# Optimization experiments

Hardware: AMD Instinct MI355X
Metric: run time of the kernel (lower is better)

## Reference

```python
import jax, jax.numpy as jnp
import numpy as np

EPS = 1e-5  # torch BatchNorm1d default eps


def setup_inputs() -> dict:
    key = jax.random.key(0)
    ks = jax.random.split(key, 8)
    F, P = 32, 64            # frames, peds per frame
    B = F * P                # batch = 2048
    E, H, M, D = 64, 128, 512, 1024  # embed, h_dim, pool_mlp_dim, bottleneck
    starts = np.arange(F, dtype=np.int64) * P
    seq_start_end = jnp.asarray(np.stack([starts, starts + P], axis=1))
    inp = {
        "curr_h_states": jax.random.normal(ks[0], (1, B, H), dtype=jnp.float32),
        "curr_pos": jax.random.normal(ks[1], (B, 2), dtype=jnp.float32),
        "seq_start_end": seq_start_end,
        # embedding: Linear(2, E)
        "We": jax.random.normal(ks[2], (2, E), dtype=jnp.float32) * 0.5,
        "be": jnp.zeros((E,), dtype=jnp.float32),
        # mlp layer 1: Linear(E+H, M) + BN(M)
        "W1": jax.random.normal(ks[3], (E + H, M), dtype=jnp.float32) * 0.05,
        "b1": jnp.zeros((M,), dtype=jnp.float32),
        "g1": jnp.ones((M,), dtype=jnp.float32),
        "beta1": jnp.zeros((M,), dtype=jnp.float32),
        # mlp layer 2: Linear(M, D) + BN(D)
        "W2": jax.random.normal(ks[4], (M, D), dtype=jnp.float32) * 0.04,
        "b2": jnp.zeros((D,), dtype=jnp.float32),
        "g2": jnp.ones((D,), dtype=jnp.float32),
        "beta2": jnp.zeros((D,), dtype=jnp.float32),
        # BN running stats (eval mode)
        "rm1": jnp.zeros((M,), dtype=jnp.float32),
        "rv1": jnp.ones((M,), dtype=jnp.float32),
        "rm2": jnp.zeros((D,), dtype=jnp.float32),
        "rv2": jnp.ones((D,), dtype=jnp.float32),
    }
    return inp


def _bn(x, g, beta, rm, rv):
    return g * (x - rm) * jax.lax.rsqrt(rv + EPS) + beta


def reference(curr_h_states, curr_pos, seq_start_end, We, be, W1, b1, g1, beta1,
              W2, b2, g2, beta2, rm1, rv1, rm2, rv2):
    # Equal-size frames: vectorize the per-frame Python loop via a reshape.
    F = seq_start_end.shape[0]
    B = curr_h_states.shape[1]
    P = B // F
    h = curr_h_states[0].reshape(F, P, -1)      # (F, P, H)
    pos = curr_pos.reshape(F, P, 2)             # (F, P, 2)
    # rel_pos[f, i, j] = pos[f, j] - pos[f, i]  (repeat minus repeat_interleave)
    rel = pos[:, None, :, :] - pos[:, :, None, :]          # (F, P, P, 2)
    emb = rel @ We + be                                     # (F, P, P, E)
    h_rep = jnp.broadcast_to(h[:, None, :, :], (F, P, P, h.shape[-1]))
    x = jnp.concatenate([emb, h_rep], axis=-1)              # (F, P, P, E+H)
    x = jax.nn.relu(_bn(x @ W1 + b1, g1, beta1, rm1, rv1))  # (F, P, P, M)
    x = jax.nn.relu(_bn(x @ W2 + b2, g2, beta2, rm2, rv2))  # (F, P, P, D)
    pool_h = x.max(axis=2)                                  # max over j -> (F, P, D)
    return pool_h.reshape(B, -1)                            # (B, D)
```

## Files before the change

kernel.cpp:

```cpp
#include <hip/hip_runtime.h>
#include <hip/hip_bf16.h>
#include <stdint.h>

#define EPS_BN 1e-5f

constexpr int Fn = 32;
constexpr int Pn = 64;
constexpr int Bn = 2048;
constexpr int Hn = 128;
constexpr int En = 64;
constexpr int Mn = 512;
constexpr int Dn = 1024;

using bf16x8 = __attribute__((ext_vector_type(8))) short;
using f32x4  = __attribute__((ext_vector_type(4))) float;

static __device__ __forceinline__ float    bcf(uint32_t u) { return __builtin_bit_cast(float, u); }
static __device__ __forceinline__ uint32_t bcu(float f)    { return __builtin_bit_cast(uint32_t, f); }
static __device__ __forceinline__ unsigned short bfbits(float f) {
  return __builtin_bit_cast(unsigned short, __float2bfloat16(f));
}

static __device__ __forceinline__ void dma16(const uint4* g, uint4* l) {
  __builtin_amdgcn_global_load_lds(
      (const __attribute__((address_space(1))) unsigned int*)g,
      (__attribute__((address_space(3))) unsigned int*)l, 16, 0, 0);
}

__global__ void prep_all(const float* __restrict__ hs, const float* __restrict__ pos,
                         const float* __restrict__ We, const float* __restrict__ be,
                         const float* __restrict__ W1, const float* __restrict__ b1,
                         const float* __restrict__ g1, const float* __restrict__ beta1,
                         const float* __restrict__ rm1, const float* __restrict__ rv1,
                         const float* __restrict__ W2, const float* __restrict__ b2,
                         const float* __restrict__ g2, const float* __restrict__ beta2,
                         const float* __restrict__ rm2, const float* __restrict__ rv2,
                         __hip_bfloat16* __restrict__ Agb, __hip_bfloat16* __restrict__ Qgb,
                         uint4* __restrict__ W2f, float* __restrict__ c2) {
  __shared__ float smem[64 * 65];
  int bid = blockIdx.x, t = threadIdx.x;
  if (bid < 256) {
    int rb = bid * 8, m = t;
    float* hsh = smem;
    float* psh = smem + 1024;
    for (int idx = t; idx < 8 * Hn; idx += 512) hsh[idx] = hs[rb * Hn + idx];
    if (t < 16) psh[t] = pos[rb * 2 + t];
    __syncthreads();
    float w0 = 0.f, w1 = 0.f, c = 0.f;
    for (int e = 0; e < En; ++e) {
      float w = W1[e * Mn + m];
      w0 += We[e] * w; w1 += We[En + e] * w; c += be[e] * w;
    }
    c += b1[m];
    float s  = g1[m] * rsqrtf(rv1[m] + EPS_BN);
    float tt = beta1[m] - rm1[m] * s;
    float acc[8];
#pragma unroll
    for (int ri = 0; ri < 8; ++ri) acc[ri] = c;
    for (int e = 0; e < Hn; ++e) {
      float w = W1[(En + e) * Mn + m];
#pragma unroll
      for (int ri = 0; ri < 8; ++ri) acc[ri] += hsh[ri * Hn + e] * w;
    }
#pragma unroll
    for (int ri = 0; ri < 8; ++ri) {
      float q = psh[ri * 2] * w0 + psh[ri * 2 + 1] * w1;
      Agb[(rb + ri) * Mn + m] = __float2bfloat16((acc[ri] + q) * s + tt);
      Qgb[(rb + ri) * Mn + m] = __float2bfloat16(q * s);
    }
  } else {
    int b2i = bid - 256;
    int d0 = (b2i & 15) * 64, k0 = (b2i >> 4) * 64;
    int col = t & 63, row8 = t >> 6;
#pragma unroll
    for (int rr = 0; rr < 8; ++rr) {
      int row = rr * 8 + row8;
      smem[row * 65 + col] = W2[(k0 + row) * Dn + d0 + col];
    }
    __syncthreads();
    int lane = t & 63, q8 = t >> 6;
    int sel = q8 & 3, kcl = q8 >> 2;
    int dl = sel * 16 + (lane & 15), d = d0 + dl;
    float sf = g2[d] * rsqrtf(rv2[d] + EPS_BN);
    int kb = kcl * 32 + (lane >> 4) * 8;
    uint32_t wd[4];
#pragma unroll
    for (int h = 0; h < 4; ++h) {
      uint32_t u0 = bfbits(smem[(kb + 2 * h) * 65 + dl] * sf);
      uint32_t u1 = bfbits(smem[(kb + 2 * h + 1) * 65 + dl] * sf);
      wd[h] = u0 | (u1 << 16);
    }
    int ntile = (d0 >> 4) + sel;
    int kc    = (k0 >> 5) + kcl;
    W2f[(ntile * 16 + kc) * 64 + lane] = (uint4){wd[0], wd[1], wd[2], wd[3]};
    if (k0 == 0 && t < 64) {
      int dd = d0 + t;
      float ss = g2[dd] * rsqrtf(rv2[dd] + EPS_BN);
      c2[dd] = b2[dd] * ss + beta2[dd] - rm2[dd] * ss;
    }
  }
}

__launch_bounds__(256, 3)
__global__ void gemm_pool(const __hip_bfloat16* __restrict__ Agb,
                          const __hip_bfloat16* __restrict__ Qgb,
                          const uint4* __restrict__ W2f,
                          const float* __restrict__ c2, float* __restrict__ out) {
  __shared__ uint4 Bs[2][512];
  __shared__ float red_s[4][2][128];

  int ct = blockIdx.x;
  int rt = blockIdx.y;
  int f = rt >> 5, i0 = (rt & 31) * 2;
  int t = threadIdx.x, lane = t & 63, w = t >> 6;

  int jr = w * 16 + (lane & 15);
  int ko = (lane >> 4) * 8;

  const uint4* aP  = (const uint4*)(Agb + (f * Pn + jr) * Mn + ko);
  const uint4* q0P = (const uint4*)(Qgb + (f * Pn + i0) * Mn + ko);
  const uint4* q1P = (const uint4*)(Qgb + (f * Pn + i0 + 1) * Mn + ko);
  const uint4* bS0 = W2f + ((ct * 8 + 2 * w) * 16) * 64 + lane;
  const uint4* bS1 = W2f + ((ct * 8 + 2 * w + 1) * 16) * 64 + lane;

  dma16(bS0, &Bs[0][(2 * w) * 64]);
  dma16(bS1, &Bs[0][(2 * w + 1) * 64]);
  uint4 rA = aP[0], rQ0 = q0P[0], rQ1 = q1P[0];

  f32x4 acc0[8], acc1[8];
#pragma unroll
  for (int nt = 0; nt < 8; ++nt) {
    acc0[nt] = (f32x4){0.f, 0.f, 0.f, 0.f};
    acc1[nt] = (f32x4){0.f, 0.f, 0.f, 0.f};
  }

#pragma unroll
  for (int kc = 0; kc < 16; ++kc) {
    int p = kc & 1;
    __syncthreads();

    bf16x8 bg[8];
#pragma unroll
    for (int nt = 0; nt < 8; ++nt)
      bg[nt] = *(const bf16x8*)&Bs[p][nt * 64 + lane];

    uint4 nA = rA, nQ0 = rQ0, nQ1 = rQ1;
    if (kc < 15) {
      dma16(bS0 + (kc + 1) * 64, &Bs[p ^ 1][(2 * w) * 64]);
      dma16(bS1 + (kc + 1) * 64, &Bs[p ^ 1][(2 * w + 1) * 64]);
      nA  = aP[(kc + 1) * 4];
      nQ0 = q0P[(kc + 1) * 4];
      nQ1 = q1P[(kc + 1) * 4];
    }

    uint4 x0, x1;
#pragma unroll
    for (int v = 0; v < 4; ++v) {
      uint32_t aw  = ((const uint32_t*)&rA)[v];
      uint32_t q0w = ((const uint32_t*)&rQ0)[v];
      uint32_t q1w = ((const uint32_t*)&rQ1)[v];
      float alo = bcf(aw << 16), ahi = bcf(aw);
      float x0lo = fmaxf(alo - bcf(q0w << 16), 0.f);
      float x0hi = fmaxf(ahi - bcf(q0w), 0.f);
      float x1lo = fmaxf(alo - bcf(q1w << 16), 0.f);
      float x1hi = fmaxf(ahi - bcf(q1w), 0.f);
      ((uint32_t*)&x0)[v] = __builtin_amdgcn_perm(bcu(x0hi), bcu(x0lo), 0x07060302u);
      ((uint32_t*)&x1)[v] = __builtin_amdgcn_perm(bcu(x1hi), bcu(x1lo), 0x07060302u);
    }
    bf16x8 af0 = __builtin_bit_cast(bf16x8, x0);
    bf16x8 af1 = __builtin_bit_cast(bf16x8, x1);

#pragma unroll
    for (int nt = 0; nt < 8; ++nt) {
      acc0[nt] = __builtin_amdgcn_mfma_f32_16x16x32_bf16(af0, bg[nt], acc0[nt], 0, 0, 0);
      acc1[nt] = __builtin_amdgcn_mfma_f32_16x16x32_bf16(af1, bg[nt], acc1[nt], 0, 0, 0);
    }
    rA = nA; rQ0 = nQ0; rQ1 = nQ1;
  }

#pragma unroll
  for (int nt = 0; nt < 8; ++nt) {
    float m0 = fmaxf(fmaxf(acc0[nt][0], acc0[nt][1]), fmaxf(acc0[nt][2], acc0[nt][3]));
    float m1 = fmaxf(fmaxf(acc1[nt][0], acc1[nt][1]), fmaxf(acc1[nt][2], acc1[nt][3]));
    m0 = fmaxf(m0, __shfl_xor(m0, 16));
    m0 = fmaxf(m0, __shfl_xor(m0, 32));
    m1 = fmaxf(m1, __shfl_xor(m1, 16));
    m1 = fmaxf(m1, __shfl_xor(m1, 32));
    if (lane < 16) {
      red_s[w][0][nt * 16 + lane] = m0;
      red_s[w][1][nt * 16 + lane] = m1;
    }
  }
  __syncthreads();
  int is = t >> 7, dl = t & 127;
  float v = fmaxf(fmaxf(red_s[0][is][dl], red_s[1][is][dl]),
                  fmaxf(red_s[2][is][dl], red_s[3][is][dl]));
  out[(f * Pn + i0 + is) * Dn + ct * 128 + dl] = fmaxf(v + c2[ct * 128 + dl], 0.f);
}

extern "C" void kernel_launch(void* const* d_in, const int* in_sizes, int n_in,
                              void* d_out, int out_size, void* d_ws, size_t ws_size,
                              hipStream_t stream) {
  const float* hs    = (const float*)d_in[0];
  const float* pos   = (const float*)d_in[1];
  const float* We    = (const float*)d_in[3];
  const float* be    = (const float*)d_in[4];
  const float* W1    = (const float*)d_in[5];
  const float* b1    = (const float*)d_in[6];
  const float* g1    = (const float*)d_in[7];
  const float* beta1 = (const float*)d_in[8];
  const float* W2    = (const float*)d_in[9];
  const float* b2    = (const float*)d_in[10];
  const float* g2    = (const float*)d_in[11];
  const float* beta2 = (const float*)d_in[12];
  const float* rm1   = (const float*)d_in[13];
  const float* rv1   = (const float*)d_in[14];
  const float* rm2   = (const float*)d_in[15];
  const float* rv2   = (const float*)d_in[16];

  char* ws = (char*)d_ws;
  float* c2 = (float*)(ws + 0);
  __hip_bfloat16* Agb = (__hip_bfloat16*)(ws + 4096);
  __hip_bfloat16* Qgb = (__hip_bfloat16*)(ws + 4096 + 2097152);
  uint4* W2f = (uint4*)(ws + 4096 + 2 * 2097152);
  float* out = (float*)d_out;

  prep_all<<<384, 512, 0, stream>>>(hs, pos, We, be, W1, b1, g1, beta1, rm1, rv1,
                                    W2, b2, g2, beta2, rm2, rv2, Agb, Qgb, W2f, c2);
  gemm_pool<<<dim3(Dn / 128, (Bn * Pn) / 128), 256, 0, stream>>>(Agb, Qgb, W2f, c2, out);
}
```

Before: 281.8 us.

## Enlarge gemm_pool tile to four query rows with half-K W2 staging in LDS

```diff
diff --git a/kernel.cpp b/kernel.cpp
--- a/kernel.cpp
+++ b/kernel.cpp
@@ -25,6 +25,18 @@
   __builtin_amdgcn_global_load_lds(
       (const __attribute__((address_space(1))) unsigned int*)g,
       (__attribute__((address_space(3))) unsigned int*)l, 16, 0, 0);
+}
+
+static __device__ __forceinline__ bf16x8 mk_af(uint4 a, uint4 q) {
+  uint4 x;
+#pragma unroll
+  for (int v = 0; v < 4; ++v) {
+    uint32_t aw = ((const uint32_t*)&a)[v], qw = ((const uint32_t*)&q)[v];
+    float lo = fmaxf(bcf(aw << 16) - bcf(qw << 16), 0.f);
+    float hi = fmaxf(bcf(aw) - bcf(qw), 0.f);
+    ((uint32_t*)&x)[v] = __builtin_amdgcn_perm(bcu(hi), bcu(lo), 0x07060302u);
+  }
+  return __builtin_bit_cast(bf16x8, x);
 }
 
 __global__ void prep_all(const float* __restrict__ hs, const float* __restrict__ pos,
@@ -101,101 +113,102 @@
   }
 }
 
-__launch_bounds__(256, 3)
+__launch_bounds__(256, 2)
 __global__ void gemm_pool(const __hip_bfloat16* __restrict__ Agb,
                           const __hip_bfloat16* __restrict__ Qgb,
                           const uint4* __restrict__ W2f,
                           const float* __restrict__ c2, float* __restrict__ out) {
-  __shared__ uint4 Bs[2][512];
-  __shared__ float red_s[4][2][128];
+  __shared__ uint4 Bs[4096];
 
   int ct = blockIdx.x;
   int rt = blockIdx.y;
-  int f = rt >> 5, i0 = (rt & 31) * 2;
+  int f = rt >> 4, i0 = (rt & 15) * 4;
+
   int t = threadIdx.x, lane = t & 63, w = t >> 6;
-
-  int jr = w * 16 + (lane & 15);
-  int ko = (lane >> 4) * 8;
-
-  const uint4* aP  = (const uint4*)(Agb + (f * Pn + jr) * Mn + ko);
-  const uint4* q0P = (const uint4*)(Qgb + (f * Pn + i0) * Mn + ko);
-  const uint4* q1P = (const uint4*)(Qgb + (f * Pn + i0 + 1) * Mn + ko);
-  const uint4* bS0 = W2f + ((ct * 8 + 2 * w) * 16) * 64 + lane;
-  const uint4* bS1 = W2f + ((ct * 8 + 2 * w + 1) * 16) * 64 + lane;
-
-  dma16(bS0, &Bs[0][(2 * w) * 64]);
-  dma16(bS1, &Bs[0][(2 * w + 1) * 64]);
-  uint4 rA = aP[0], rQ0 = q0P[0], rQ1 = q1P[0];
-
-  f32x4 acc0[8], acc1[8];
-#pragma unroll
-  for (int nt = 0; nt < 8; ++nt) {
-    acc0[nt] = (f32x4){0.f, 0.f, 0.f, 0.f};
-    acc1[nt] = (f32x4){0.f, 0.f, 0.f, 0.f};
-  }
-
-#pragma unroll
-  for (int kc = 0; kc < 16; ++kc) {
-    int p = kc & 1;
+  int jw = w & 1, dw = w >> 1;
+  int dw4 = dw * 4;
+
+  int jr0 = 32 * jw + (lane & 15);
+  int ko  = (lane >> 4) * 8;
+
+  const uint4* aP0 = (const uint4*)(Agb + (f * Pn + jr0) * Mn + ko);
+  const uint4* aP1 = (const uint4*)(Agb + (f * Pn + jr0 + 16) * Mn + ko);
+  const uint4* qP0 = (const uint4*)(Qgb + (f * Pn + i0 + 0) * Mn + ko);
+  const uint4* qP1 = (const uint4*)(Qgb + (f * Pn + i0 + 1) * Mn + ko);
+  const uint4* qP2 = (const uint4*)(Qgb + (f * Pn + i0 + 2) * Mn + ko);
+  const uint4* qP3 = (const uint4*)(Qgb + (f * Pn + i0 + 3) * Mn + ko);
+  const uint4* W2base = W2f + (size_t)(ct * 8) * 16 * 64 + lane;
+
+  f32x4 acc[4][2][4];
+#pragma unroll
+  for (int i = 0; i < 4; ++i)
+#pragma unroll
+    for (int mt = 0; mt < 2; ++mt)
+#pragma unroll
+      for (int nt = 0; nt < 4; ++nt) acc[i][mt][nt] = (f32x4){0.f, 0.f, 0.f, 0.f};
+
+  uint4 rA0 = aP0[0], rA1 = aP1[0];
+  uint4 rQ0 = qP0[0], rQ1 = qP1[0], rQ2 = qP2[0], rQ3 = qP3[0];
+
+  for (int ph = 0; ph < 2; ++ph) {
+    if (ph) __syncthreads();
+#pragma unroll
+    for (int s = 0; s < 16; ++s) {
+      int idx = w * 16 + s;
+      int kc8 = idx >> 3, gnt = idx & 7;
+      dma16(W2base + (gnt * 16 + ph * 8 + kc8) * 64, Bs + idx * 64);
+    }
     __syncthreads();
 
-    bf16x8 bg[8];
-#pragma unroll
-    for (int nt = 0; nt < 8; ++nt)
-      bg[nt] = *(const bf16x8*)&Bs[p][nt * 64 + lane];
-
-    uint4 nA = rA, nQ0 = rQ0, nQ1 = rQ1;
-    if (kc < 15) {
-      dma16(bS0 + (kc + 1) * 64, &Bs[p ^ 1][(2 * w) * 64]);
-      dma16(bS1 + (kc + 1) * 64, &Bs[p ^ 1][(2 * w + 1) * 64]);
-      nA  = aP[(kc + 1) * 4];
-      nQ0 = q0P[(kc + 1) * 4];
-      nQ1 = q1P[(kc + 1) * 4];
-    }
-
-    uint4 x0, x1;
-#pragma unroll
-    for (int v = 0; v < 4; ++v) {
-      uint32_t aw  = ((const uint32_t*)&rA)[v];
-      uint32_t q0w = ((const uint32_t*)&rQ0)[v];
-      uint32_t q1w = ((const uint32_t*)&rQ1)[v];
-      float alo = bcf(aw << 16), ahi = bcf(aw);
-      float x0lo = fmaxf(alo - bcf(q0w << 16), 0.f);
-      float x0hi = fmaxf(ahi - bcf(q0w), 0.f);
-      float x1lo = fmaxf(alo - bcf(q1w << 16), 0.f);
-      float x1hi = fmaxf(ahi - bcf(q1w), 0.f);
-      ((uint32_t*)&x0)[v] = __builtin_amdgcn_perm(bcu(x0hi), bcu(x0lo), 0x07060302u);
-      ((uint32_t*)&x1)[v] = __builtin_amdgcn_perm(bcu(x1hi), bcu(x1lo), 0x07060302u);
-    }
-    bf16x8 af0 = __builtin_bit_cast(bf16x8, x0);
-    bf16x8 af1 = __builtin_bit_cast(bf16x8, x1);
-
-#pragma unroll
-    for (int nt = 0; nt < 8; ++nt) {
-      acc0[nt] = __builtin_amdgcn_mfma_f32_16x16x32_bf16(af0, bg[nt], acc0[nt], 0, 0, 0);
-      acc1[nt] = __builtin_amdgcn_mfma_f32_16x16x32_bf16(af1, bg[nt], acc1[nt], 0, 0, 0);
-    }
-    rA = nA; rQ0 = nQ0; rQ1 = nQ1;
-  }
-
-#pragma unroll
-  for (int nt = 0; nt < 8; ++nt) {
-    float m0 = fmaxf(fmaxf(acc0[nt][0], acc0[nt][1]), fmaxf(acc0[nt][2], acc0[nt][3]));
-    float m1 = fmaxf(fmaxf(acc1[nt][0], acc1[nt][1]), fmaxf(acc1[nt][2], acc1[nt][3]));
-    m0 = fmaxf(m0, __shfl_xor(m0, 16));
-    m0 = fmaxf(m0, __shfl_xor(m0, 32));
-    m1 = fmaxf(m1, __shfl_xor(m1, 16));
-    m1 = fmaxf(m1, __shfl_xor(m1, 32));
-    if (lane < 16) {
-      red_s[w][0][nt * 16 + lane] = m0;
-      red_s[w][1][nt * 16 + lane] = m1;
-    }
-  }
+    for (int kc8 = 0; kc8 < 8; ++kc8) {
+      int kc = ph * 8 + kc8;
+      bf16x8 bg[4];
+#pragma unroll
+      for (int nt = 0; nt < 4; ++nt)
+        bg[nt] = *(const bf16x8*)(Bs + (kc8 * 8 + dw4 + nt) * 64 + lane);
+
+      int kn = (kc < 15) ? kc + 1 : 15;
+      uint4 nA0 = aP0[kn * 4], nA1 = aP1[kn * 4];
+      uint4 nQ0 = qP0[kn * 4], nQ1 = qP1[kn * 4];
+      uint4 nQ2 = qP2[kn * 4], nQ3 = qP3[kn * 4];
+
+#pragma unroll
+      for (int i = 0; i < 4; ++i) {
+        uint4 q = (i == 0) ? rQ0 : (i == 1) ? rQ1 : (i == 2) ? rQ2 : rQ3;
+        bf16x8 af0 = mk_af(rA0, q);
+        bf16x8 af1 = mk_af(rA1, q);
+#pragma unroll
+        for (int nt = 0; nt < 4; ++nt) {
+          acc[i][0][nt] = __builtin_amdgcn_mfma_f32_16x16x32_bf16(af0, bg[nt], acc[i][0][nt], 0, 0, 0);
+          acc[i][1][nt] = __builtin_amdgcn_mfma_f32_16x16x32_bf16(af1, bg[nt], acc[i][1][nt], 0, 0, 0);
+        }
+      }
+      rA0 = nA0; rA1 = nA1;
+      rQ0 = nQ0; rQ1 = nQ1; rQ2 = nQ2; rQ3 = nQ3;
+    }
+  }
+
   __syncthreads();
-  int is = t >> 7, dl = t & 127;
-  float v = fmaxf(fmaxf(red_s[0][is][dl], red_s[1][is][dl]),
-                  fmaxf(red_s[2][is][dl], red_s[3][is][dl]));
-  out[(f * Pn + i0 + is) * Dn + ct * 128 + dl] = fmaxf(v + c2[ct * 128 + dl], 0.f);
+  float* redf = (float*)Bs;
+#pragma unroll
+  for (int i = 0; i < 4; ++i) {
+#pragma unroll
+    for (int nt = 0; nt < 4; ++nt) {
+      f32x4 a0 = acc[i][0][nt], a1 = acc[i][1][nt];
+      float mx = fmaxf(fmaxf(fmaxf(a0[0], a0[1]), fmaxf(a0[2], a0[3])),
+                       fmaxf(fmaxf(a1[0], a1[1]), fmaxf(a1[2], a1[3])));
+      mx = fmaxf(mx, __shfl_xor(mx, 16));
+      mx = fmaxf(mx, __shfl_xor(mx, 32));
+      if (lane < 16) redf[(jw * 4 + i) * 128 + dw * 64 + nt * 16 + lane] = mx;
+    }
+  }
+  __syncthreads();
+#pragma unroll
+  for (int r = t; r < 512; r += 256) {
+    int i = r >> 7, d = r & 127;
+    float v = fmaxf(redf[i * 128 + d], redf[(4 + i) * 128 + d]);
+    out[(f * Pn + i0 + i) * Dn + ct * 128 + d] = fmaxf(v + c2[ct * 128 + d], 0.f);
+  }
 }
 
 extern "C" void kernel_launch(void* const* d_in, const int* in_sizes, int n_in,
@@ -227,5 +240,5 @@
 
   prep_all<<<384, 512, 0, stream>>>(hs, pos, We, be, W1, b1, g1, beta1, rm1, rv1,
                                     W2, b2, g2, beta2, rm2, rv2, Agb, Qgb, W2f, c2);
-  gemm_pool<<<dim3(Dn / 128, (Bn * Pn) / 128), 256, 0, stream>>>(Agb, Qgb, W2f, c2, out);
-}
+  gemm_pool<<<dim3(Dn / 128, (Fn * Pn * Pn) / 256), 256, 0, stream>>>(Agb, Qgb, W2f, c2, out);
+}
```

Result: faster. 268.5 us (-4.7%).
